# Performance work log

Measured on AMD Instinct MI355X. Metric: run time of the kernel, lower is better.

The kernel has to match this reference:

```python
import jax, jax.numpy as jnp
import numpy as np

BS, BT, DIM = 32, 1024, 512
NEG_MASK = -1000000.0  # masked_fill value for b/i scores
NEG_SPAN = -1000.0     # lower-triangle fill for span matrix


def setup_inputs() -> dict:
    key = jax.random.key(0)
    ks = jax.random.split(key, 6)
    s = 1.0 / np.sqrt(DIM)  # xavier-ish scale
    return {
        "x": jax.random.normal(ks[0], (BS, DIM), jnp.float32),
        "sen_vecs": jax.random.normal(ks[1], (BS, BT, DIM), jnp.float32),
        "sen_mask": jnp.ones((BS, BT), jnp.int32),
        "Wb": jax.random.normal(ks[2], (DIM, DIM), jnp.float32) * s,
        "bb": jnp.zeros((DIM,), jnp.float32),
        "Wi": jax.random.normal(ks[3], (DIM, DIM), jnp.float32) * s,
        "bi": jnp.zeros((DIM,), jnp.float32),
        "Wo": jax.random.normal(ks[4], (DIM, DIM), jnp.float32) * s,
        "bo": jnp.zeros((DIM,), jnp.float32),
    }


def reference(x, sen_vecs, sen_mask, Wb, bb, Wi, bi, Wo, bo):
    def proj_scores(W, b):
        # torch Linear: sen_vecs @ W.T + b, then dot with x -> [bs, bt]
        h = jnp.einsum('btd,ed->bte', sen_vecs, W) + b
        return jnp.einsum('bte,be->bt', h, x)

    m0 = (sen_mask == 0)
    sb = jnp.where(m0, NEG_MASK, proj_scores(Wb, bb))  # [bs,bt]
    si = jnp.where(m0, NEG_MASK, proj_scores(Wi, bi))
    so = jnp.where(m0, 0.0, proj_scores(Wo, bo))

    # per-step logsumexp over the 3 BIO labels; the CRF-style recursions
    # f[t] = lse(f[t-1] + bio[t-1]) collapse to cumsums since f[t-1] is scalar.
    lse = jax.nn.logsumexp(jnp.stack([sb, si, so], axis=-1), axis=-1)  # [bs,bt]
    z = jnp.zeros((sb.shape[0], 1), sb.dtype)
    fwd = jnp.concatenate([z, jnp.cumsum(lse, axis=1)], axis=1)                      # [bs,bt+1]
    bwd = jnp.concatenate([jnp.flip(jnp.cumsum(jnp.flip(lse, 1), 1), 1), z], axis=1)  # [bs,bt+1]
    full = fwd[:, -1:]

    # prefix sums of scores_i: Ci[t] = sum(si[:t]); sum(si[s:e]) = Ci[e]-Ci[s]
    Ci = jnp.concatenate([z, jnp.cumsum(si, axis=1)], axis=1)  # [bs,bt+1]

    A = sb + fwd[:, :-1] - Ci[:, :-1] - full   # indexed by span start s
    B = Ci[:, :-1] + bwd[:, 1:] + so           # indexed by span end e
    span = A[:, :, None] + B[:, None, :]       # [bs, bt, bt], rows=s, cols=e
    tri = jnp.triu(jnp.ones((sb.shape[1], sb.shape[1]), bool))  # e >= s
    return jnp.where(tri[None], span, jnp.asarray(NEG_SPAN, span.dtype))
```

## Files before the change

kernel.cpp:

```cpp
#include <hip/hip_runtime.h>
#include <math.h>


#define BS 32
#define BT 1024
#define DIM 512
#define NEG_MASK -1000000.0f
#define NEG_SPAN -1000.0f

__global__ __launch_bounds__(256) void k1_proj(
    const float* __restrict__ x,
    const float* __restrict__ Wb, const float* __restrict__ bb,
    const float* __restrict__ Wi, const float* __restrict__ bi,
    const float* __restrict__ Wo, const float* __restrict__ bo,
    float* __restrict__ Y, float* __restrict__ C)
{
    const int w = blockIdx.y;
    const float* __restrict__ W    = (w == 0) ? Wb : (w == 1) ? Wi : Wo;
    const float* __restrict__ bias = (w == 0) ? bb : (w == 1) ? bi : bo;
    const int tid = threadIdx.x;

    if (blockIdx.x == 8) {
        const int v = tid >> 6, l = tid & 63;
        for (int b = v; b < BS; b += 4) {
            float acc = 0.f;
            for (int e = l; e < DIM; e += 64) acc += bias[e] * x[b * DIM + e];
            #pragma unroll
            for (int o = 32; o >= 1; o >>= 1) acc += __shfl_xor(acc, o);
            if (l == 0) C[w * BS + b] = acc;
        }
        return;
    }

    __shared__ float xs[BS * DIM];
    for (int k = tid; k < BS * DIM; k += 256) xs[k] = x[k];
    __syncthreads();

    const int d0 = blockIdx.x * 64;
    const int dt = tid & 63, bg = tid >> 6;
    const int d  = d0 + dt;

    float acc[8];
    #pragma unroll
    for (int i = 0; i < 8; i++) acc[i] = 0.f;
    for (int e = 0; e < DIM; e++) {
        const float wv = W[e * DIM + d];
        #pragma unroll
        for (int i = 0; i < 8; i++)
            acc[i] += wv * xs[(bg * 8 + i) * DIM + e];
    }
    #pragma unroll
    for (int i = 0; i < 8; i++)
        Y[w * BS * DIM + (bg * 8 + i) * DIM + d] = acc[i];
}

__global__ __launch_bounds__(256) void k2a_scores(
    const float* __restrict__ sv, const int* __restrict__ mask,
    const float* __restrict__ Y, const float* __restrict__ C,
    float* __restrict__ SB, float* __restrict__ SI, float* __restrict__ SO,
    float* __restrict__ LSE)
{
    __shared__ float ys[3 * DIM];
    const int blk = blockIdx.x;
    const int b   = blk >> 8;
    const int t0  = (blk & 255) * 4;
    const int tid = threadIdx.x;

    for (int k = tid; k < 3 * DIM; k += 256) {
        const int w = k >> 9, d = k & (DIM - 1);
        ys[k] = Y[w * BS * DIM + b * DIM + d];
    }
    __syncthreads();

    const int v = tid >> 6, l = tid & 63;
    const int t = t0 + v;

    const float4* __restrict__ yb4 = (const float4*)(ys);
    const float4* __restrict__ yi4 = (const float4*)(ys + DIM);
    const float4* __restrict__ yo4 = (const float4*)(ys + 2 * DIM);
    const float4* __restrict__ svp =
        (const float4*)(sv + (size_t)(b * BT + t) * DIM);

    const float4 s1 = svp[l];
    const float4 s2 = svp[64 + l];

    float4 y1, y2;
    y1 = yb4[l]; y2 = yb4[64 + l];
    float aB = s1.x*y1.x + s1.y*y1.y + s1.z*y1.z + s1.w*y1.w
             + s2.x*y2.x + s2.y*y2.y + s2.z*y2.z + s2.w*y2.w;
    y1 = yi4[l]; y2 = yi4[64 + l];
    float aI = s1.x*y1.x + s1.y*y1.y + s1.z*y1.z + s1.w*y1.w
             + s2.x*y2.x + s2.y*y2.y + s2.z*y2.z + s2.w*y2.w;
    y1 = yo4[l]; y2 = yo4[64 + l];
    float aO = s1.x*y1.x + s1.y*y1.y + s1.z*y1.z + s1.w*y1.w
             + s2.x*y2.x + s2.y*y2.y + s2.z*y2.z + s2.w*y2.w;

    #pragma unroll
    for (int o = 32; o >= 1; o >>= 1) {
        aB += __shfl_xor(aB, o);
        aI += __shfl_xor(aI, o);
        aO += __shfl_xor(aO, o);
    }

    if (l == 0) {
        float sb = aB + C[0 * BS + b];
        float si = aI + C[1 * BS + b];
        float so = aO + C[2 * BS + b];
        if (mask[b * BT + t] == 0) { sb = NEG_MASK; si = NEG_MASK; so = 0.f; }
        const float m   = fmaxf(sb, fmaxf(si, so));
        const float lse = m + logf(expf(sb - m) + expf(si - m) + expf(so - m));
        const int idx = b * BT + t;
        SB[idx] = sb; SI[idx] = si; SO[idx] = so; LSE[idx] = lse;
    }
}

__global__ __launch_bounds__(1024) void k2b_scan(
    const float* __restrict__ SB, const float* __restrict__ SI,
    const float* __restrict__ SO, const float* __restrict__ LSE,
    float* __restrict__ A, float* __restrict__ Bv)
{
    __shared__ float sL[BT], sS[BT];
    const int b = blockIdx.x, t = threadIdx.x;
    const float l0 = LSE[b * BT + t];
    const float s0 = SI[b * BT + t];
    sL[t] = l0; sS[t] = s0;
    __syncthreads();

    for (int off = 1; off < BT; off <<= 1) {
        float a = 0.f, c = 0.f;
        if (t >= off) { a = sL[t - off]; c = sS[t - off]; }
        __syncthreads();
        if (t >= off) { sL[t] += a; sS[t] += c; }
        __syncthreads();
    }

    const float total = sL[BT - 1];
    const float pl = sL[t] - l0;
    const float ps = sS[t] - s0;
    A [b * BT + t] = SB[b * BT + t] + pl - ps - total;
    Bv[b * BT + t] = ps + (total - sL[t]) + SO[b * BT + t];
}

__global__ __launch_bounds__(256) void k3_span(
    const float* __restrict__ A, const float* __restrict__ Bv,
    float4* __restrict__ out)
{
    const int idx = blockIdx.x * 256 + threadIdx.x;
    const int b  = idx >> 18;
    const int r  = idx & 0x3FFFF;
    const int i  = r >> 8;
    const int j4 = r & 255;

    const float a = A[b * BT + i];
    const float4 bb4 = ((const float4*)(Bv + b * BT))[j4];
    const int j = j4 * 4;
    float4 o;
    o.x = (j     >= i) ? a + bb4.x : NEG_SPAN;
    o.y = (j + 1 >= i) ? a + bb4.y : NEG_SPAN;
    o.z = (j + 2 >= i) ? a + bb4.z : NEG_SPAN;
    o.w = (j + 3 >= i) ? a + bb4.w : NEG_SPAN;
    out[idx] = o;
}

extern "C" void kernel_launch(void* const* d_in, const int* in_sizes, int n_in,
                              void* d_out, int out_size, void* d_ws, size_t ws_size,
                              hipStream_t stream) {
    const float* x   = (const float*)d_in[0];
    const float* sv  = (const float*)d_in[1];
    const int*   msk = (const int*)  d_in[2];
    const float* Wb  = (const float*)d_in[3];
    const float* bb  = (const float*)d_in[4];
    const float* Wi  = (const float*)d_in[5];
    const float* bi  = (const float*)d_in[6];
    const float* Wo  = (const float*)d_in[7];
    const float* bo  = (const float*)d_in[8];

    float* ws = (float*)d_ws;
    float* Y   = ws;
    float* C   = ws + 49152;
    float* SB  = ws + 49664;
    float* SI  = SB + BS * BT;
    float* SO  = SI + BS * BT;
    float* LSE = SO + BS * BT;
    float* A   = LSE + BS * BT;
    float* Bv  = A + BS * BT;

    k1_proj  <<<dim3(9, 3), 256, 0, stream>>>(x, Wb, bb, Wi, bi, Wo, bo, Y, C);
    k2a_scores<<<BS * 256, 256, 0, stream>>>(sv, msk, Y, C, SB, SI, SO, LSE);
    k2b_scan <<<BS, 1024, 0, stream>>>(SB, SI, SO, LSE, A, Bv);
    k3_span  <<<32768, 256, 0, stream>>>(A, Bv, (float4*)d_out);
}
```

Before: 272.8 us.

## Use nontemporal loads/stores for streaming data and wave-shuffle scan

Marks the single-use sen_vecs reads in the score kernel and the large span-matrix writes as nontemporal, so streaming traffic is meant to bypass cache retention. The per-batch prefix scan is rewritten from a shared-memory Hillis-Steele loop with many block barriers into a wave-level shuffle scan plus a 16-entry cross-wave combine, with a single barrier. The nontemporal hints may help or hurt depending on how the hardware handles them, and the scan kernel is a small share of total time.

Measured after the change: 276.2 us. Within noise of the previous version (+1.2%).

```diff
diff --git a/kernel.cpp b/kernel.cpp
--- a/kernel.cpp
+++ b/kernel.cpp
@@ -7,6 +7,8 @@
 #define DIM 512
 #define NEG_MASK -1000000.0f
 #define NEG_SPAN -1000.0f
+
+typedef float vf4 __attribute__((ext_vector_type(4)));
 
 __global__ __launch_bounds__(256) void k1_proj(
     const float* __restrict__ x,
@@ -75,16 +77,16 @@
     const int v = tid >> 6, l = tid & 63;
     const int t = t0 + v;
 
-    const float4* __restrict__ yb4 = (const float4*)(ys);
-    const float4* __restrict__ yi4 = (const float4*)(ys + DIM);
-    const float4* __restrict__ yo4 = (const float4*)(ys + 2 * DIM);
-    const float4* __restrict__ svp =
-        (const float4*)(sv + (size_t)(b * BT + t) * DIM);
-
-    const float4 s1 = svp[l];
-    const float4 s2 = svp[64 + l];
-
-    float4 y1, y2;
+    const vf4* __restrict__ yb4 = (const vf4*)(ys);
+    const vf4* __restrict__ yi4 = (const vf4*)(ys + DIM);
+    const vf4* __restrict__ yo4 = (const vf4*)(ys + 2 * DIM);
+    const vf4* __restrict__ svp =
+        (const vf4*)(sv + (size_t)(b * BT + t) * DIM);
+
+    const vf4 s1 = __builtin_nontemporal_load(&svp[l]);
+    const vf4 s2 = __builtin_nontemporal_load(&svp[64 + l]);
+
+    vf4 y1, y2;
     y1 = yb4[l]; y2 = yb4[64 + l];
     float aB = s1.x*y1.x + s1.y*y1.y + s1.z*y1.z + s1.w*y1.w
              + s2.x*y2.x + s2.y*y2.y + s2.z*y2.z + s2.w*y2.w;
@@ -119,31 +121,42 @@
     const float* __restrict__ SO, const float* __restrict__ LSE,
     float* __restrict__ A, float* __restrict__ Bv)
 {
-    __shared__ float sL[BT], sS[BT];
+    __shared__ float wL[16], wS[16];
     const int b = blockIdx.x, t = threadIdx.x;
+    const int wave = t >> 6, lane = t & 63;
+
     const float l0 = LSE[b * BT + t];
     const float s0 = SI[b * BT + t];
-    sL[t] = l0; sS[t] = s0;
+
+    float l = l0, s = s0;
+    #pragma unroll
+    for (int off = 1; off <= 32; off <<= 1) {
+        const float lu = __shfl_up(l, off);
+        const float su = __shfl_up(s, off);
+        if (lane >= off) { l += lu; s += su; }
+    }
+    if (lane == 63) { wL[wave] = l; wS[wave] = s; }
     __syncthreads();
 
-    for (int off = 1; off < BT; off <<= 1) {
-        float a = 0.f, c = 0.f;
-        if (t >= off) { a = sL[t - off]; c = sS[t - off]; }
-        __syncthreads();
-        if (t >= off) { sL[t] += a; sS[t] += c; }
-        __syncthreads();
-    }
-
-    const float total = sL[BT - 1];
-    const float pl = sL[t] - l0;
-    const float ps = sS[t] - s0;
-    A [b * BT + t] = SB[b * BT + t] + pl - ps - total;
-    Bv[b * BT + t] = ps + (total - sL[t]) + SO[b * BT + t];
+    float offL = 0.f, offS = 0.f, totL = 0.f;
+    #pragma unroll
+    for (int w = 0; w < 16; w++) {
+        const float a = wL[w], c = wS[w];
+        if (w < wave) { offL += a; offS += c; }
+        totL += a;
+    }
+    const float inclL = l + offL;
+    const float inclS = s + offS;
+
+    const float pl = inclL - l0;
+    const float ps = inclS - s0;
+    A [b * BT + t] = SB[b * BT + t] + pl - ps - totL;
+    Bv[b * BT + t] = ps + (totL - inclL) + SO[b * BT + t];
 }
 
 __global__ __launch_bounds__(256) void k3_span(
     const float* __restrict__ A, const float* __restrict__ Bv,
-    float4* __restrict__ out)
+    vf4* __restrict__ out)
 {
     const int idx = blockIdx.x * 256 + threadIdx.x;
     const int b  = idx >> 18;
@@ -152,14 +165,14 @@
     const int j4 = r & 255;
 
     const float a = A[b * BT + i];
-    const float4 bb4 = ((const float4*)(Bv + b * BT))[j4];
+    const vf4 bb4 = ((const vf4*)(Bv + b * BT))[j4];
     const int j = j4 * 4;
-    float4 o;
+    vf4 o;
     o.x = (j     >= i) ? a + bb4.x : NEG_SPAN;
     o.y = (j + 1 >= i) ? a + bb4.y : NEG_SPAN;
     o.z = (j + 2 >= i) ? a + bb4.z : NEG_SPAN;
     o.w = (j + 3 >= i) ? a + bb4.w : NEG_SPAN;
-    out[idx] = o;
+    __builtin_nontemporal_store(o, &out[idx]);
 }
 
 extern "C" void kernel_launch(void* const* d_in, const int* in_sizes, int n_in,
@@ -188,5 +201,5 @@
     k1_proj  <<<dim3(9, 3), 256, 0, stream>>>(x, Wb, bb, Wi, bi, Wo, bo, Y, C);
     k2a_scores<<<BS * 256, 256, 0, stream>>>(sv, msk, Y, C, SB, SI, SO, LSE);
     k2b_scan <<<BS, 1024, 0, stream>>>(SB, SI, SO, LSE, A, Bv);
-    k3_span  <<<32768, 256, 0, stream>>>(A, Bv, (float4*)d_out);
-}
+    k3_span  <<<32768, 256, 0, stream>>>(A, Bv, (vf4*)d_out);
+}
```
